# Performance work log

Hardware: AMD Instinct MI355X
Metric: run time of the kernel (lower is better)

The kernel has to match this reference:

```python
import jax, jax.numpy as jnp
import numpy as np
import math

L, E, H, T, V, B = 8, 1024, 16, 1024, 32000, 2
HD = E // H
EPS = 1e-5


def _quantize_sym(key, shape, std=0.02):
    w = std * jax.random.normal(key, shape, jnp.float32)
    s = jnp.max(jnp.abs(w)) / 127.0  # symmetric int8: 2**(8-1)-1
    q = jnp.clip(jnp.round(w / s), -128, 127).astype(jnp.int8)
    return q, s


def setup_inputs() -> dict:
    key = jax.random.key(0)
    ks = iter(jax.random.split(key, 64 + 16 * L))
    idx = jax.random.randint(next(ks), (B, T), 0, V)
    tok_emb = 0.02 * jax.random.normal(next(ks), (V, E), jnp.float32)
    pos_emb = 0.02 * jax.random.normal(next(ks), (T, E), jnp.float32)
    # per-layer stacked params
    attn_qw, attn_s = [], []
    aproj_qw, aproj_s = [], []
    fc_qw, fc_s = [], []
    mproj_qw, mproj_s = [], []
    for _ in range(L):
        q, s = _quantize_sym(next(ks), (3 * E, E)); attn_qw.append(q); attn_s.append(s)
        q, s = _quantize_sym(next(ks), (E, E)); aproj_qw.append(q); aproj_s.append(s)
        q, s = _quantize_sym(next(ks), (4 * E, E)); fc_qw.append(q); fc_s.append(s)
        q, s = _quantize_sym(next(ks), (E, 4 * E)); mproj_qw.append(q); mproj_s.append(s)
    lm_qw, lm_s = _quantize_sym(next(ks), (V, E))
    return {
        "idx": idx,
        "tok_emb": tok_emb,
        "pos_emb": pos_emb,
        "ln1_g": jnp.ones((L, E)), "ln1_b": jnp.zeros((L, E)),
        "attn_qw": jnp.stack(attn_qw), "attn_s": jnp.stack(attn_s), "attn_b": jnp.zeros((L, 3 * E)),
        "aproj_qw": jnp.stack(aproj_qw), "aproj_s": jnp.stack(aproj_s), "aproj_b": jnp.zeros((L, E)),
        "ln2_g": jnp.ones((L, E)), "ln2_b": jnp.zeros((L, E)),
        "fc_qw": jnp.stack(fc_qw), "fc_s": jnp.stack(fc_s), "fc_b": jnp.zeros((L, 4 * E)),
        "mproj_qw": jnp.stack(mproj_qw), "mproj_s": jnp.stack(mproj_s), "mproj_b": jnp.zeros((L, E)),
        "lnf_g": jnp.ones((E,)), "lnf_b": jnp.zeros((E,)),
        "lm_qw": lm_qw, "lm_s": lm_s,
    }


def _dequant(q, s):
    return q.astype(jnp.float32) * s


def _layernorm(x, g, b):
    m = jnp.mean(x, axis=-1, keepdims=True)
    v = jnp.mean(jnp.square(x - m), axis=-1, keepdims=True)
    return (x - m) * jax.lax.rsqrt(v + EPS) * g + b


def _gpt_forward(idx, tok_emb, pos_emb, ln1_g, ln1_b, attn_qw, attn_s, attn_b,
                 aproj_qw, aproj_s, aproj_b, ln2_g, ln2_b, fc_qw, fc_s, fc_b,
                 mproj_qw, mproj_s, mproj_b, lnf_g, lnf_b, lm_qw, lm_s):
    x = tok_emb[idx] + pos_emb[None, :, :]  # [B,T,E]
    causal = jnp.tril(jnp.ones((T, T), dtype=bool))  # [T,T]
    scale = 1.0 / math.sqrt(HD)

    def block(x, p):
        (l1g, l1b, aqw, asc, ab, pqw, psc, pb,
         l2g, l2b, fqw, fsc, fb, mqw, msc, mb) = p
        h = _layernorm(x, l1g, l1b)
        qkv = h @ _dequant(aqw, asc).T + ab  # [B,T,3E]
        q, k, v = jnp.split(qkv, 3, axis=-1)
        q = q.reshape(B, T, H, HD).transpose(0, 2, 1, 3)  # [B,H,T,HD]
        k = k.reshape(B, T, H, HD).transpose(0, 2, 1, 3)
        v = v.reshape(B, T, H, HD).transpose(0, 2, 1, 3)
        att = jnp.einsum('bhqd,bhkd->bhqk', q, k) * scale
        att = jnp.where(causal, att, -jnp.inf)
        att = jax.nn.softmax(att, axis=-1)
        y = jnp.einsum('bhqk,bhkd->bhqd', att, v)
        y = y.transpose(0, 2, 1, 3).reshape(B, T, E)
        y = y @ _dequant(pqw, psc).T + pb
        x = x + y
        h = _layernorm(x, l2g, l2b)
        h = jax.nn.gelu(h @ _dequant(fqw, fsc).T + fb, approximate=False)
        x = x + h @ _dequant(mqw, msc).T + mb
        return x, None

    layer_params = (ln1_g, ln1_b, attn_qw, attn_s, attn_b,
                    aproj_qw, aproj_s, aproj_b, ln2_g, ln2_b,
                    fc_qw, fc_s, fc_b, mproj_qw, mproj_s, mproj_b)
    x, _ = jax.lax.scan(block, x, layer_params)
    x = _layernorm(x, lnf_g, lnf_b)
    logits = x @ _dequant(lm_qw, lm_s).T  # [B,T,V], no bias
    return logits


def reference(idx, tok_emb, pos_emb, ln1_g, ln1_b, attn_qw, attn_s, attn_b,
              aproj_qw, aproj_s, aproj_b, ln2_g, ln2_b, fc_qw, fc_s, fc_b,
              mproj_qw, mproj_s, mproj_b, lnf_g, lnf_b, lm_qw, lm_s):
    return _gpt_forward(idx, tok_emb, pos_emb, ln1_g, ln1_b, attn_qw, attn_s, attn_b,
                        aproj_qw, aproj_s, aproj_b, ln2_g, ln2_b, fc_qw, fc_s, fc_b,
                        mproj_qw, mproj_s, mproj_b, lnf_g, lnf_b, lm_qw, lm_s)
```

## Files before the change

### kernel.cpp

```cpp
#include <hip/hip_runtime.h>
#include <math.h>

typedef _Float16 h16;
typedef __attribute__((ext_vector_type(8))) _Float16 half8;
typedef __attribute__((ext_vector_type(4))) _Float16 half4;
typedef __attribute__((ext_vector_type(4))) float f32x4;

#define DEVI static __device__ __forceinline__

constexpr int LAY = 8, E = 1024, NH = 16, T = 1024, VOC = 32000, BATCH = 2, HD = 64;
constexpr int MROWS = BATCH * T;
constexpr int E2 = E * E;

DEVI void glds16(const void* g, void* l) {
  __builtin_amdgcn_global_load_lds((const __attribute__((address_space(1))) void*)g,
                                   (__attribute__((address_space(3))) void*)l, 16, 0, 0);
}

__global__ __launch_bounds__(256) void prep_stride_k(const unsigned char* __restrict__ qw1,
                                                     const unsigned char* __restrict__ qw2,
                                                     int* __restrict__ stridew) {
  __shared__ int red2[4], red4[4];
  const int tid = threadIdx.x;
  const int NB = 8192;
  int c2 = 0, c4 = 0;
  for (int i = tid; i < NB; i += 256) {
    const unsigned char b1 = qw1[i], b2 = qw2[i];
    const int s1 = (b1 == 0x00 || b1 == 0xFF) ? 1 : 0;
    const int s2 = (b2 == 0x00 || b2 == 0xFF) ? 1 : 0;
    if (i & 1) c2 += s1 + s2;
    if (i & 3) c4 += s1 + s2;
  }
#pragma unroll
  for (int d = 32; d >= 1; d >>= 1) { c2 += __shfl_xor(c2, d); c4 += __shfl_xor(c4, d); }
  if ((tid & 63) == 0) { red2[tid >> 6] = c2; red4[tid >> 6] = c4; }
  __syncthreads();
  if (tid == 0) {
    const int t2 = red2[0] + red2[1] + red2[2] + red2[3];
    const int t4 = red4[0] + red4[1] + red4[2] + red4[3];
    int stride = 1;
    if (t4 > (NB * 3 / 2) * 98 / 100) stride = 4;
    else if (t2 > NB * 98 / 100) stride = 2;
    stridew[0] = stride;
  }
}

DEVI half8 dq8(const signed char* src, int bstr, float s) {
  half8 o;
  if (bstr == 4) {
    int4 r0 = *reinterpret_cast<const int4*>(src);
    int4 r1 = *reinterpret_cast<const int4*>(src + 16);
    const int* c0 = reinterpret_cast<const int*>(&r0);
    const int* c1 = reinterpret_cast<const int*>(&r1);
#pragma unroll
    for (int j = 0; j < 4; ++j) o[j] = (h16)((float)c0[j] * s);
#pragma unroll
    for (int j = 0; j < 4; ++j) o[4 + j] = (h16)((float)c1[j] * s);
  } else if (bstr == 2) {
    int4 r0 = *reinterpret_cast<const int4*>(src);
    const short* c0 = reinterpret_cast<const short*>(&r0);
#pragma unroll
    for (int j = 0; j < 8; ++j) o[j] = (h16)((float)c0[j] * s);
  } else {
    int2 r0 = *reinterpret_cast<const int2*>(src);
    const signed char* c0 = reinterpret_cast<const signed char*>(&r0);
#pragma unroll
    for (int j = 0; j < 8; ++j) o[j] = (h16)((float)c0[j] * s);
  }
  return o;
}

__global__ __launch_bounds__(256) void dequant_all_k(const signed char* __restrict__ q,
                                                     const int* __restrict__ strideptr,
                                                     const float* __restrict__ sp, int P,
                                                     h16* __restrict__ out, int n) {
  const int i = (blockIdx.x * 256 + threadIdx.x) * 8;
  if (i >= n) return;
  const float s = sp[i / P];
  const int bstr = strideptr[0];
  *reinterpret_cast<half8*>(out + i) = dq8(q + (size_t)i * (size_t)bstr, bstr, s);
}

__global__ __launch_bounds__(256) void dequant_layer_k(
    const signed char* __restrict__ qkv_q, const signed char* __restrict__ ap_q,
    const signed char* __restrict__ fc_q, const signed char* __restrict__ mp_q,
    const float* __restrict__ qkv_s, const float* __restrict__ ap_s,
    const float* __restrict__ fc_s, const float* __restrict__ mp_s, int l,
    const int* __restrict__ strideptr,
    h16* __restrict__ wq, h16* __restrict__ wa, h16* __restrict__ wf,
    h16* __restrict__ wm) {
  const int e = (blockIdx.x * 256 + threadIdx.x) * 8;
  const int bstr = strideptr[0];
  const signed char* src;
  h16* dst;
  float s;
  if (e < 3 * E2) {
    src = qkv_q + ((size_t)l * 3 * E2 + e) * (size_t)bstr;
    dst = wq + e;
    s = qkv_s[l];
  } else if (e < 4 * E2) {
    const int e2 = e - 3 * E2;
    src = ap_q + ((size_t)l * E2 + e2) * (size_t)bstr;
    dst = wa + e2;
    s = ap_s[l];
  } else if (e < 8 * E2) {
    const int e2 = e - 4 * E2;
    src = fc_q + ((size_t)l * 4 * E2 + e2) * (size_t)bstr;
    dst = wf + e2;
    s = fc_s[l];
  } else {
    const int e2 = e - 8 * E2;
    src = mp_q + ((size_t)l * 4 * E2 + e2) * (size_t)bstr;
    dst = wm + e2;
    s = mp_s[l];
  }
  *reinterpret_cast<half8*>(dst) = dq8(src, bstr, s);
}

__global__ __launch_bounds__(256) void embed_k(const int* __restrict__ idx,
                                               const float* __restrict__ tok,
                                               const float* __restrict__ pos,
                                               float* __restrict__ x) {
  const int row = blockIdx.x;
  const int t = row & (T - 1);
  const int id = idx[row];
  const float4 a = reinterpret_cast<const float4*>(tok + (size_t)id * E)[threadIdx.x];
  const float4 p = reinterpret_cast<const float4*>(pos + (size_t)t * E)[threadIdx.x];
  float4 o; o.x = a.x + p.x; o.y = a.y + p.y; o.z = a.z + p.z; o.w = a.w + p.w;
  reinterpret_cast<float4*>(x + (size_t)row * E)[threadIdx.x] = o;
}

__global__ __launch_bounds__(256) void ln_k(const float* __restrict__ x,
                                            const float* __restrict__ g,
                                            const float* __restrict__ bb,
                                            h16* __restrict__ out) {
  __shared__ float red[8];
  const int row = blockIdx.x, tid = threadIdx.x;
  const float4 v = reinterpret_cast<const float4*>(x + (size_t)row * E)[tid];
  float s1 = v.x + v.y + v.z + v.w;
  float s2 = v.x * v.x + v.y * v.y + v.z * v.z + v.w * v.w;
#pragma unroll
  for (int d = 32; d >= 1; d >>= 1) { s1 += __shfl_xor(s1, d); s2 += __shfl_xor(s2, d); }
  if ((tid & 63) == 0) { red[tid >> 6] = s1; red[4 + (tid >> 6)] = s2; }
  __syncthreads();
  s1 = red[0] + red[1] + red[2] + red[3];
  s2 = red[4] + red[5] + red[6] + red[7];
  const float mean = s1 * (1.0f / E);
  const float var = s2 * (1.0f / E) - mean * mean;
  const float rstd = rsqrtf(var + 1e-5f);
  const float4 gv = reinterpret_cast<const float4*>(g)[tid];
  const float4 bv = reinterpret_cast<const float4*>(bb)[tid];
  half4 o;
  o[0] = (h16)((v.x - mean) * rstd * gv.x + bv.x);
  o[1] = (h16)((v.y - mean) * rstd * gv.y + bv.y);
  o[2] = (h16)((v.z - mean) * rstd * gv.z + bv.z);
  o[3] = (h16)((v.w - mean) * rstd * gv.w + bv.w);
  *reinterpret_cast<half4*>(out + (size_t)row * E + tid * 4) = o;
}

__global__ __launch_bounds__(256) void reduce_ln_k(const float* __restrict__ pbuf, int S,
                                                   const float* __restrict__ bias,
                                                   float* __restrict__ x,
                                                   const float* __restrict__ g,
                                                   const float* __restrict__ bb,
                                                   h16* __restrict__ out) {
  __shared__ float red[8];
  const int row = blockIdx.x, tid = threadIdx.x;
  const size_t base = (size_t)row * E + tid * 4;
  float4 a = *reinterpret_cast<const float4*>(pbuf + base);
  for (int s = 1; s < S; ++s) {
    const float4 p = *reinterpret_cast<const float4*>(pbuf + (size_t)s * MROWS * E + base);
    a.x += p.x; a.y += p.y; a.z += p.z; a.w += p.w;
  }
  const float4 bv0 = *reinterpret_cast<const float4*>(bias + tid * 4);
  float4 v = *reinterpret_cast<const float4*>(x + base);
  v.x += a.x + bv0.x; v.y += a.y + bv0.y; v.z += a.z + bv0.z; v.w += a.w + bv0.w;
  *reinterpret_cast<float4*>(x + base) = v;
  float s1 = v.x + v.y + v.z + v.w;
  float s2 = v.x * v.x + v.y * v.y + v.z * v.z + v.w * v.w;
#pragma unroll
  for (int d = 32; d >= 1; d >>= 1) { s1 += __shfl_xor(s1, d); s2 += __shfl_xor(s2, d); }
  if ((tid & 63) == 0) { red[tid >> 6] = s1; red[4 + (tid >> 6)] = s2; }
  __syncthreads();
  s1 = red[0] + red[1] + red[2] + red[3];
  s2 = red[4] + red[5] + red[6] + red[7];
  const float mean = s1 * (1.0f / E);
  const float var = s2 * (1.0f / E) - mean * mean;
  const float rstd = rsqrtf(var + 1e-5f);
  const float4 gv = *reinterpret_cast<const float4*>(g + tid * 4);
  const float4 lb = *reinterpret_cast<const float4*>(bb + tid * 4);
  half4 o;
  o[0] = (h16)((v.x - mean) * rstd * gv.x + lb.x);
  o[1] = (h16)((v.y - mean) * rstd * gv.y + lb.y);
  o[2] = (h16)((v.z - mean) * rstd * gv.z + lb.z);
  o[3] = (h16)((v.w - mean) * rstd * gv.w + lb.w);
  *reinterpret_cast<half4*>(out + (size_t)row * E + tid * 4) = o;
}

template <int OUT_KIND, int DO_GELU, int DO_RESID>
__global__ __launch_bounds__(256) void gemm_bt(const h16* __restrict__ A,
                                               const h16* __restrict__ Bw,
                                               const float* __restrict__ bias,
                                               const float* __restrict__ resid,
                                               void* __restrict__ Cout,
                                               int M, int N, int K, int ldc) {
  __shared__ __align__(16) h16 As[2][4096];
  __shared__ __align__(16) h16 Bs[2][4096];
  const int tid = threadIdx.x;
  const int w = tid >> 6, lane = tid & 63;
  const int lin = blockIdx.x;
  const int cpx = gridDim.x >> 3;
  const int swz = (lin & 7) * cpx + (lin >> 3);
  const int m0 = (swz & 15) << 7;
  const int n0 = (swz >> 4) << 7;
  const int wr = w >> 1, wc = w & 1;
  const int lr = lane >> 2, lc8 = (lane & 3) << 3;
  const h16* gA = A + (size_t)(m0 + w * 16 + lr) * K + lc8;
  const h16* gB = Bw + (size_t)(n0 + w * 16 + lr) * K + lc8;
  f32x4 acc[4][4] = {};
  const int fl = lane & 15, fk = (lane >> 4) << 3;
  const int nk = K >> 5;
  auto stage = [&](int buf, int kt) {
    const h16* pa = gA + (kt << 5);
    const h16* pb = gB + (kt << 5);
    glds16(pa, &As[buf][w * 512]);
    glds16(pa + (size_t)64 * K, &As[buf][2048 + w * 512]);
    glds16(pb, &Bs[buf][w * 512]);
    glds16(pb + (size_t)64 * K, &Bs[buf][2048 + w * 512]);
  };
  stage(0, 0);
  __syncthreads();
  int cur = 0;
  for (int kt = 0; kt < nk; ++kt) {
    if (kt + 1 < nk) stage(cur ^ 1, kt + 1);
    half8 af[4], bfr[4];
#pragma unroll
    for (int mi = 0; mi < 4; ++mi)
      af[mi] = *reinterpret_cast<const half8*>(&As[cur][(wr * 64 + mi * 16 + fl) * 32 + fk]);
#pragma unroll
    for (int ni = 0; ni < 4; ++ni)
      bfr[ni] = *reinterpret_cast<const half8*>(&Bs[cur][(wc * 64 + ni * 16 + fl) * 32 + fk]);
#pragma unroll
    for (int mi = 0; mi < 4; ++mi)
#pragma unroll
      for (int ni = 0; ni < 4; ++ni)
        acc[mi][ni] = __builtin_amdgcn_mfma_f32_16x16x32_f16(af[mi], bfr[ni], acc[mi][ni], 0, 0, 0);
    __syncthreads();
    cur ^= 1;
  }
  const int fr4 = (lane >> 4) << 2;
#pragma unroll
  for (int mi = 0; mi < 4; ++mi) {
#pragma unroll
    for (int ni = 0; ni < 4; ++ni) {
      const int col = n0 + wc * 64 + ni * 16 + fl;
      const float bv = bias ? bias[col] : 0.0f;
#pragma unroll
      for (int j = 0; j < 4; ++j) {
        const int row = m0 + wr * 64 + mi * 16 + fr4 + j;
        float v = acc[mi][ni][j] + bv;
        if (DO_GELU) v = 0.5f * v * (1.0f + erff(v * 0.70710678118f));
        if (DO_RESID) v += resid[(size_t)row * ldc + col];
        if (OUT_KIND == 1)
          reinterpret_cast<h16*>(Cout)[(size_t)row * ldc + col] = (h16)v;
        else
          reinterpret_cast<float*>(Cout)[(size_t)row * ldc + col] = v;
      }
    }
  }
}

__global__ __launch_bounds__(512) void gemm_bt256(const h16* __restrict__ A,
                                                  const h16* __restrict__ Bw,
                                                  float* __restrict__ Cout,
                                                  int M, int N, int K) {
  __shared__ __align__(16) h16 As[2][8192];
  __shared__ __align__(16) h16 Bs[2][8192];
  const int tid = threadIdx.x;
  const int w = tid >> 6, lane = tid & 63;
  const int lin = blockIdx.x;
  const int cpx = gridDim.x >> 3;
  const int swz = (lin & 7) * cpx + (lin >> 3);
  const int m0 = (swz & 7) << 8;
  const int n0 = (swz >> 3) << 8;
  const int wr = w >> 2, wc = w & 3;
  const int lr = lane >> 2, lc8 = (lane & 3) << 3;
  const h16* gA = A + (size_t)(m0 + w * 16 + lr) * K + lc8;
  const h16* gB = Bw + (size_t)(n0 + w * 16 + lr) * K + lc8;
  f32x4 acc[8][4] = {};
  const int fl = lane & 15, fk = (lane >> 4) << 3;
  const int nk = K >> 5;
  auto stage = [&](int buf, int kt) {
    const h16* pa = gA + (kt << 5);
    const h16* pb = gB + (kt << 5);
    glds16(pa, &As[buf][w * 512]);
    glds16(pa + (size_t)128 * K, &As[buf][4096 + w * 512]);
    glds16(pb, &Bs[buf][w * 512]);
    glds16(pb + (size_t)128 * K, &Bs[buf][4096 + w * 512]);
  };
  stage(0, 0);
  __syncthreads();
  int cur = 0;
  for (int kt = 0; kt < nk; ++kt) {
    if (kt + 1 < nk) stage(cur ^ 1, kt + 1);
    half8 af[8], bfr[4];
#pragma unroll
    for (int mi = 0; mi < 8; ++mi)
      af[mi] = *reinterpret_cast<const half8*>(&As[cur][(wr * 128 + mi * 16 + fl) * 32 + fk]);
#pragma unroll
    for (int ni = 0; ni < 4; ++ni)
      bfr[ni] = *reinterpret_cast<const half8*>(&Bs[cur][(wc * 64 + ni * 16 + fl) * 32 + fk]);
#pragma unroll
    for (int mi = 0; mi < 8; ++mi)
#pragma unroll
      for (int ni = 0; ni < 4; ++ni)
        acc[mi][ni] = __builtin_amdgcn_mfma_f32_16x16x32_f16(af[mi], bfr[ni], acc[mi][ni], 0, 0, 0);
    __syncthreads();
    cur ^= 1;
  }
  const int fr4 = (lane >> 4) << 2;
#pragma unroll
  for (int mi = 0; mi < 8; ++mi)
#pragma unroll
    for (int ni = 0; ni < 4; ++ni) {
      const int col = n0 + wc * 64 + ni * 16 + fl;
#pragma unroll
      for (int j = 0; j < 4; ++j) {
        const int row = m0 + wr * 128 + mi * 16 + fr4 + j;
        Cout[(size_t)row * N + col] = acc[mi][ni][j];
      }
    }
}

__global__ __launch_bounds__(256) void gemm_btk(const h16* __restrict__ A,
                                                const h16* __restrict__ Bw,
                                                float* __restrict__ pbuf,
                                                int M, int N, int Kc, int ldk) {
  __shared__ __align__(16) h16 As[2][4096];
  __shared__ __align__(16) h16 Bs[2][4096];
  const int tid = threadIdx.x;
  const int w = tid >> 6, lane = tid & 63;
  const int lin = blockIdx.x;
  const int cpx = gridDim.x >> 3;
  const int swz = (lin & 7) * cpx + (lin >> 3);
  const int m0 = (swz & 15) << 7;
  const int n0 = (swz >> 4) << 7;
  const int s = blockIdx.y;
  const int koff = s * Kc;
  const int wr = w >> 1, wc = w & 1;
  const int lr = lane >> 2, lc8 = (lane & 3) << 3;
  const h16* gA = A + (size_t)(m0 + w * 16 + lr) * ldk + koff + lc8;
  const h16* gB = Bw + (size_t)(n0 + w * 16 + lr) * ldk + koff + lc8;
  f32x4 acc[4][4] = {};
  const int fl = lane & 15, fk = (lane >> 4) << 3;
  const int nk = Kc >> 5;
  auto stage = [&](int buf, int kt) {
    const h16* pa = gA + (kt << 5);
    const h16* pb = gB + (kt << 5);
    glds16(pa, &As[buf][w * 512]);
    glds16(pa + (size_t)64 * ldk, &As[buf][2048 + w * 512]);
    glds16(pb, &Bs[buf][w * 512]);
    glds16(pb + (size_t)64 * ldk, &Bs[buf][2048 + w * 512]);
  };
  stage(0, 0);
  __syncthreads();
  int cur = 0;
  for (int kt = 0; kt < nk; ++kt) {
    if (kt + 1 < nk) stage(cur ^ 1, kt + 1);
    half8 af[4], bfr[4];
#pragma unroll
    for (int mi = 0; mi < 4; ++mi)
      af[mi] = *reinterpret_cast<const half8*>(&As[cur][(wr * 64 + mi * 16 + fl) * 32 + fk]);
#pragma unroll
    for (int ni = 0; ni < 4; ++ni)
      bfr[ni] = *reinterpret_cast<const half8*>(&Bs[cur][(wc * 64 + ni * 16 + fl) * 32 + fk]);
#pragma unroll
    for (int mi = 0; mi < 4; ++mi)
#pragma unroll
      for (int ni = 0; ni < 4; ++ni)
        acc[mi][ni] = __builtin_amdgcn_mfma_f32_16x16x32_f16(af[mi], bfr[ni], acc[mi][ni], 0, 0, 0);
    __syncthreads();
    cur ^= 1;
  }
  float* out = pbuf + (size_t)s * M * N;
  const int fr4 = (lane >> 4) << 2;
#pragma unroll
  for (int mi = 0; mi < 4; ++mi)
#pragma unroll
    for (int ni = 0; ni < 4; ++ni) {
      const int col = n0 + wc * 64 + ni * 16 + fl;
#pragma unroll
      for (int j = 0; j < 4; ++j) {
        const int row = m0 + wr * 64 + mi * 16 + fr4 + j;
        out[(size_t)row * N + col] = acc[mi][ni][j];
      }
    }
}

__global__ __launch_bounds__(256) void attn_k(const h16* __restrict__ qkv,
                                              h16* __restrict__ yout) {
  __shared__ __align__(16) h16 Ks[2][4096];
  __shared__ __align__(16) h16 VTs[2][4096];
  __shared__ __align__(16) h16 Ps[4096];
  const int qt = (int)gridDim.x - 1 - (int)blockIdx.x;
  const int bh = blockIdx.y;
  const int b = bh >> 4, h = bh & 15;
  const int tid = threadIdx.x, w = tid >> 6, lane = tid & 63;
  const int fl = lane & 15, fkg = lane >> 4, fk = fkg << 3;
  const size_t rowQ0 = (size_t)b * T + qt * 64 + w * 16;
  const h16* qbase = qkv + (rowQ0 + fl) * 3072 + h * 64;
  const half8 qf0 = *reinterpret_cast<const half8*>(qbase + fk);
  const half8 qf1 = *reinterpret_cast<const half8*>(qbase + 32 + fk);
  f32x4 yacc[4] = {};
  float m_run[4], l_run[4];
#pragma unroll
  for (int j = 0; j < 4; ++j) { m_run[j] = -1e30f; l_run[j] = 0.f; }
  const int q_g0 = qt * 64 + w * 16 + (fkg << 2);
  const int krow = lane >> 3, kcol8 = (lane & 7) << 3;
  const int vrow = tid >> 2, vcol8 = (tid & 3) << 3;

  auto stageK = [&](int kt, int buf) {
    const size_t kbase = (size_t)b * T + kt * 64;
    const h16* gk = qkv + (kbase + w * 8 + krow) * 3072 + E + h * 64 + kcol8;
    glds16(gk, &Ks[buf][w * 512]);
    glds16(gk + (size_t)32 * 3072, &Ks[buf][2048 + w * 512]);
  };
  auto loadV = [&](int kt, int half32) {
    const size_t kbase = (size_t)b * T + kt * 64;
    return *reinterpret_cast<const half8*>(qkv + (kbase + vrow) * 3072 + 2 * E + h * 64 +
                                           vcol8 + half32);
  };
  auto scatterV = [&](int buf, half8 v0, half8 v1) {
#pragma unroll
    for (int e = 0; e < 8; ++e) VTs[buf][(vcol8 + e) * 64 + vrow] = v0[e];
#pragma unroll
    for (int e = 0; e < 8; ++e) VTs[buf][(vcol8 + 32 + e) * 64 + vrow] = v1[e];
  };

  stageK(0, 0);
  {
    half8 v0 = loadV(0, 0), v1 = loadV(0, 32);
    scatterV(0, v0, v1);
  }
  __syncthreads();
  int cur = 0;
  for (int kt = 0; kt <= qt; ++kt) {
    const bool hn = kt < qt;
    half8 nv0, nv1;
    if (hn) {
      stageK(kt + 1, cur ^ 1);
      nv0 = loadV(kt + 1, 0);
      nv1 = loadV(kt + 1, 32);
    }
    f32x4 sacc[4];
#pragma unroll
    for (int ni = 0; ni < 4; ++ni) {
      const half8 kb0 = *reinterpret_cast<const half8*>(&Ks[cur][(ni * 16 + fl) * 64 + fk]);
      const half8 kb1 = *reinterpret_cast<const half8*>(&Ks[cur][(ni * 16 + fl) * 64 + 32 + fk]);
      f32x4 z = {0.f, 0.f, 0.f, 0.f};
      z = __builtin_amdgcn_mfma_f32_16x16x32_f16(qf0, kb0, z, 0, 0, 0);
      z = __builtin_amdgcn_mfma_f32_16x16x32_f16(qf1, kb1, z, 0, 0, 0);
      sacc[ni] = z;
    }
    float tmax[4] = {-1e30f, -1e30f, -1e30f, -1e30f};
#pragma unroll
    for (int ni = 0; ni < 4; ++ni) {
      const int kcol = kt * 64 + ni * 16 + fl;
#pragma unroll
      for (int j = 0; j < 4; ++j) {
        float sv = sacc[ni][j] * 0.125f;
        sv = (kcol > q_g0 + j) ? -1e30f : sv;
        sacc[ni][j] = sv;
        tmax[j] = fmaxf(tmax[j], sv);
      }
    }
#pragma unroll
    for (int d = 1; d < 16; d <<= 1) {
#pragma unroll
      for (int j = 0; j < 4; ++j) tmax[j] = fmaxf(tmax[j], __shfl_xor(tmax[j], d));
    }
    float sc_old[4], psum[4] = {0.f, 0.f, 0.f, 0.f};
#pragma unroll
    for (int j = 0; j < 4; ++j) {
      const float mn = fmaxf(m_run[j], tmax[j]);
      sc_old[j] = __expf(m_run[j] - mn);
      m_run[j] = mn;
    }
#pragma unroll
    for (int ni = 0; ni < 4; ++ni)
#pragma unroll
      for (int j = 0; j < 4; ++j) {
        const float p = __expf(sacc[ni][j] - m_run[j]);
        sacc[ni][j] = p;
        psum[j] += p;
      }
#pragma unroll
    for (int d = 1; d < 16; d <<= 1) {
#pragma unroll
      for (int j = 0; j < 4; ++j) psum[j] += __shfl_xor(psum[j], d);
    }
#pragma unroll
    for (int j = 0; j < 4; ++j) l_run[j] = l_run[j] * sc_old[j] + psum[j];
#pragma unroll
    for (int di = 0; di < 4; ++di)
#pragma unroll
      for (int j = 0; j < 4; ++j) yacc[di][j] *= sc_old[j];
    if (hn) scatterV(cur ^ 1, nv0, nv1);
#pragma unroll
    for (int ni = 0; ni < 4; ++ni)
#pragma unroll
      for (int j = 0; j < 4; ++j)
        Ps[w * 1024 + ((fkg << 2) + j) * 64 + ni * 16 + fl] = (h16)sacc[ni][j];
    __syncthreads();
    const half8 pa0 = *reinterpret_cast<const half8*>(&Ps[w * 1024 + fl * 64 + fk]);
    const half8 pa1 = *reinterpret_cast<const half8*>(&Ps[w * 1024 + fl * 64 + 32 + fk]);
#pragma unroll
    for (int di = 0; di < 4; ++di) {
      const half8 vb0 = *reinterpret_cast<const half8*>(&VTs[cur][(di * 16 + fl) * 64 + fk]);
      const half8 vb1 = *reinterpret_cast<const half8*>(&VTs[cur][(di * 16 + fl) * 64 + 32 + fk]);
      yacc[di] = __builtin_amdgcn_mfma_f32_16x16x32_f16(pa0, vb0, yacc[di], 0, 0, 0);
      yacc[di] = __builtin_amdgcn_mfma_f32_16x16x32_f16(pa1, vb1, yacc[di], 0, 0, 0);
    }
    __syncthreads();
    cur ^= 1;
  }
  float rl[4];
#pragma unroll
  for (int j = 0; j < 4; ++j) rl[j] = 1.0f / l_run[j];
  const size_t orow0 = rowQ0 + (fkg << 2);
#pragma unroll
  for (int di = 0; di < 4; ++di)
#pragma unroll
    for (int j = 0; j < 4; ++j)
      yout[(orow0 + j) * E + h * 64 + di * 16 + fl] = (h16)(yacc[di][j] * rl[j]);
}

extern "C" void kernel_launch(void* const* d_in, const int* in_sizes, int n_in,
                              void* d_out, int out_size, void* d_ws, size_t ws_size,
                              hipStream_t stream) {
  (void)in_sizes; (void)n_in; (void)out_size; (void)ws_size;
  const int* idx = (const int*)d_in[0];
  const float* tok = (const float*)d_in[1];
  const float* pos = (const float*)d_in[2];
  const float* ln1g = (const float*)d_in[3];
  const float* ln1b = (const float*)d_in[4];
  const signed char* attn_qw = (const signed char*)d_in[5];
  const float* attn_s = (const float*)d_in[6];
  const float* attn_b = (const float*)d_in[7];
  const signed char* aproj_qw = (const signed char*)d_in[8];
  const float* aproj_s = (const float*)d_in[9];
  const float* aproj_b = (const float*)d_in[10];
  const float* ln2g = (const float*)d_in[11];
  const float* ln2b = (const float*)d_in[12];
  const signed char* fc_qw = (const signed char*)d_in[13];
  const float* fc_s = (const float*)d_in[14];
  const float* fc_b = (const float*)d_in[15];
  const signed char* mproj_qw = (const signed char*)d_in[16];
  const float* mproj_s = (const float*)d_in[17];
  const float* mproj_b = (const float*)d_in[18];
  const float* lnfg = (const float*)d_in[19];
  const float* lnfb = (const float*)d_in[20];
  const signed char* lm_qw = (const signed char*)d_in[21];
  const float* lm_s = (const float*)d_in[22];

  char* ws = (char*)d_ws;
  size_t off = 0;
  auto alloc = [&](size_t bytes) {
    char* p = ws + off;
    off += (bytes + 255) & ~(size_t)255;
    return p;
  };
  float* x = (float*)alloc((size_t)MROWS * E * 4);
  h16* hbuf = (h16*)alloc((size_t)MROWS * E * 2);
  h16* big = (h16*)alloc((size_t)MROWS * 4 * E * 2);
  h16* wq = (h16*)alloc((size_t)3 * E2 * 2);
  h16* wa = (h16*)alloc((size_t)E2 * 2);
  h16* wf = (h16*)alloc((size_t)4 * E2 * 2);
  h16* wm = (h16*)alloc((size_t)4 * E2 * 2);
  float* pbuf = (float*)alloc((size_t)4 * MROWS * E * 4);
  h16* wlm = (h16*)alloc((size_t)VOC * E * 2);
  int* stridew = (int*)alloc(256);
  h16* qkvb = big;
  h16* yb = hbuf;
  h16* hfc = big;

  prep_stride_k<<<1, 256, 0, stream>>>((const unsigned char*)attn_qw,
                                       (const unsigned char*)fc_qw, stridew);
  dequant_all_k<<<VOC * E / 2048, 256, 0, stream>>>(lm_qw, stridew, lm_s, VOC * E,
                                                    wlm, VOC * E);
  embed_k<<<MROWS, 256, 0, stream>>>(idx, tok, pos, x);
  ln_k<<<MROWS, 256, 0, stream>>>(x, ln1g, ln1b, hbuf);

  for (int l = 0; l < LAY; ++l) {
    dequant_layer_k<<<12 * E2 / 2048, 256, 0, stream>>>(
        attn_qw, aproj_qw, fc_qw, mproj_qw, attn_s, aproj_s, fc_s, mproj_s, l,
        stridew, wq, wa, wf, wm);
    gemm_bt<1, 0, 0><<<24 * 16, 256, 0, stream>>>(hbuf, wq, attn_b + l * 3 * E, nullptr,
                                                  qkvb, MROWS, 3 * E, E, 3 * E);
    attn_k<<<dim3(16, 32), 256, 0, stream>>>(qkvb, yb);
    gemm_btk<<<dim3(128, 2), 256, 0, stream>>>(yb, wa, pbuf, MROWS, E, 512, E);
    reduce_ln_k<<<MROWS, 256, 0, stream>>>(pbuf, 2, aproj_b + l * E, x,
                                           ln2g + l * E, ln2b + l * E, hbuf);
    gemm_bt<1, 1, 0><<<32 * 16, 256, 0, stream>>>(hbuf, wf, fc_b + l * 4 * E, nullptr,
                                                  hfc, MROWS, 4 * E, E, 4 * E);
    gemm_btk<<<dim3(128, 4), 256, 0, stream>>>(hfc, wm, pbuf, MROWS, E, 1024, 4 * E);
    const float* ng = (l < LAY - 1) ? (ln1g + (l + 1) * E) : lnfg;
    const float* nb = (l < LAY - 1) ? (ln1b + (l + 1) * E) : lnfb;
    reduce_ln_k<<<MROWS, 256, 0, stream>>>(pbuf, 4, mproj_b + l * E, x, ng, nb, hbuf);
  }
  gemm_bt256<<<1000, 512, 0, stream>>>(hbuf, wlm, (float*)d_out, MROWS, VOC, E);
}
```

Baseline: 1.807 ms.

## Split GEMM k-step into two halves with deeper B prefetch and explicit waits

Reworks the main loop of the f16 GEMM that writes fp32 output. Each k-tile is now processed as two 4x4 MFMA half-steps. A is prefetched one tile ahead and B two tiles ahead into the slot that has just been freed. `__syncthreads` is replaced with raw `s_waitcnt vmcnt`/`lgkmcnt` and `s_barrier`, plus `sched_barrier` and `s_setprio` around the MFMA blocks. The goal is to hide global-to-LDS latency behind compute and cut register pressure from 8 to 4 A fragments. The cost is hand-managed wait counts that depend on exactly how many loads each tile issues.

```diff
diff --git a/kernel.cpp b/kernel.cpp
--- a/kernel.cpp
+++ b/kernel.cpp
@@ -290,32 +290,59 @@
   f32x4 acc[8][4] = {};
   const int fl = lane & 15, fk = (lane >> 4) << 3;
   const int nk = K >> 5;
-  auto stage = [&](int buf, int kt) {
-    const h16* pa = gA + (kt << 5);
-    const h16* pb = gB + (kt << 5);
-    glds16(pa, &As[buf][w * 512]);
-    glds16(pa + (size_t)128 * K, &As[buf][4096 + w * 512]);
-    glds16(pb, &Bs[buf][w * 512]);
-    glds16(pb + (size_t)128 * K, &Bs[buf][4096 + w * 512]);
-  };
-  stage(0, 0);
-  __syncthreads();
+  auto stageA = [&](int buf, int kt, int half) {
+    glds16(gA + (size_t)(kt << 5) + (size_t)half * 128 * K,
+           &As[buf][half * 4096 + w * 512]);
+  };
+  auto stageB = [&](int buf, int kt, int half) {
+    glds16(gB + (size_t)(kt << 5) + (size_t)half * 128 * K,
+           &Bs[buf][half * 4096 + w * 512]);
+  };
+  stageA(0, 0, 0); stageA(0, 0, 1);
+  stageB(0, 0, 0); stageB(0, 0, 1);
+  stageB(1, 1, 0); stageB(1, 1, 1);
+  asm volatile("s_waitcnt vmcnt(2)" ::: "memory");
+  asm volatile("s_barrier" ::: "memory");
   int cur = 0;
   for (int kt = 0; kt < nk; ++kt) {
-    if (kt + 1 < nk) stage(cur ^ 1, kt + 1);
-    half8 af[8], bfr[4];
-#pragma unroll
-    for (int mi = 0; mi < 8; ++mi)
+    half8 af[4], bfr[4];
+#pragma unroll
+    for (int mi = 0; mi < 4; ++mi)
       af[mi] = *reinterpret_cast<const half8*>(&As[cur][(wr * 128 + mi * 16 + fl) * 32 + fk]);
 #pragma unroll
     for (int ni = 0; ni < 4; ++ni)
       bfr[ni] = *reinterpret_cast<const half8*>(&Bs[cur][(wc * 64 + ni * 16 + fl) * 32 + fk]);
-#pragma unroll
-    for (int mi = 0; mi < 8; ++mi)
+    if (kt + 1 < nk) { stageA(cur ^ 1, kt + 1, 0); stageA(cur ^ 1, kt + 1, 1); }
+    asm volatile("s_waitcnt lgkmcnt(0)" ::: "memory");
+    __builtin_amdgcn_sched_barrier(0);
+    __builtin_amdgcn_s_setprio(1);
+#pragma unroll
+    for (int mi = 0; mi < 4; ++mi)
 #pragma unroll
       for (int ni = 0; ni < 4; ++ni)
         acc[mi][ni] = __builtin_amdgcn_mfma_f32_16x16x32_f16(af[mi], bfr[ni], acc[mi][ni], 0, 0, 0);
-    __syncthreads();
+    __builtin_amdgcn_s_setprio(0);
+    asm volatile("s_barrier" ::: "memory");
+#pragma unroll
+    for (int mi = 0; mi < 4; ++mi)
+      af[mi] = *reinterpret_cast<const half8*>(
+          &As[cur][(wr * 128 + 64 + mi * 16 + fl) * 32 + fk]);
+    if (kt + 2 < nk) { stageB(cur, kt + 2, 0); stageB(cur, kt + 2, 1); }
+    if (kt < nk - 2)
+      asm volatile("s_waitcnt vmcnt(2)" ::: "memory");
+    else
+      asm volatile("s_waitcnt vmcnt(0)" ::: "memory");
+    asm volatile("s_waitcnt lgkmcnt(0)" ::: "memory");
+    __builtin_amdgcn_sched_barrier(0);
+    __builtin_amdgcn_s_setprio(1);
+#pragma unroll
+    for (int mi = 0; mi < 4; ++mi)
+#pragma unroll
+      for (int ni = 0; ni < 4; ++ni)
+        acc[4 + mi][ni] =
+            __builtin_amdgcn_mfma_f32_16x16x32_f16(af[mi], bfr[ni], acc[4 + mi][ni], 0, 0, 0);
+    __builtin_amdgcn_s_setprio(0);
+    asm volatile("s_barrier" ::: "memory");
     cur ^= 1;
   }
   const int fr4 = (lane >> 4) << 2;
```

Result: faster. 1.748 ms (-3.3%).
